# Optimization experiments

Hardware: AMD Instinct MI355X
Metric: run time of the kernel (lower is better)

Reference implementation:

```python
import jax, jax.numpy as jnp
import numpy as np

T = 1_000_000          # number of t_eval points (~1 year at 30 s)
N_ROOMS = 10
N = 12                 # 2 latent wall nodes + n_rooms
DT = 30.0              # seconds between t_eval points
LOAD_SCALE = 50.0      # physical_cooling_scaling: W/m^2 scale for sigmoid(loads)


def setup_inputs() -> dict:
    key = jax.random.key(0)
    k1, k2, k3, k4, k5 = jax.random.split(key, 5)
    t_eval = jnp.arange(T, dtype=jnp.float32) * DT
    x0 = 26.0 * jnp.ones((N,), jnp.float32)  # reset_iv: 26 C at every node
    # Stable slow RC dynamics: negative-definite-ish A with small coupling
    A = (-1e-5 * jnp.eye(N, dtype=jnp.float32)
         + 1e-6 * jax.random.normal(k1, (N, N), jnp.float32))
    B = 1e-6 * jax.random.normal(k2, (N, 1 + N_ROOMS), jnp.float32)
    Tout_data = 10.0 + 20.0 * jax.random.uniform(k3, (T,), jnp.float32)  # outdoor temp samples on t_eval grid
    loads_raw = jax.random.normal(k4, (2, N_ROOMS), jnp.float32)         # pre-sigmoid [cool; gain] loads
    room_areas = 10.0 + 40.0 * jax.random.uniform(k5, (N_ROOMS,), jnp.float32)
    return {"t_eval": t_eval, "x0": x0, "A": A, "B": B,
            "Tout_data": Tout_data, "loads_raw": loads_raw, "room_areas": room_areas}


def reference(t_eval, x0, A, B, Tout_data, loads_raw, room_areas):
    # transform + physical scaling of loads (self.transform = sigmoid)
    loads = jax.nn.sigmoid(loads_raw) * LOAD_SCALE
    cool_load, gain_load = loads[0], loads[1]
    action = 0.0  # no cooling policy -> self.action stays 0
    Q_area = -cool_load * action + gain_load            # [n_rooms]
    Q_watts = Q_area * room_areas                        # proportional_heating
    # u = [Tout; Q_watts] so B@u = B[:,0]*Tout + B[:,1:]@Q_watts (Q constant over t)
    b0 = B[:, 0]                                         # [N]
    Bq = B[:, 1:] @ Q_watts                              # [N], constant forcing
    h = t_eval[1] - t_eval[0]                            # uniform step
    # Linear interp of Tout: value at t_i, midpoint t_i+h/2, and t_{i+1}
    To_t = Tout_data[:-1]
    To_n = Tout_data[1:]
    To_m = 0.5 * (To_t + To_n)

    def f(x, To):  # dy/dt = A x + B u
        return A @ x + b0 * To + Bq

    def step(x, tou):
        to_t, to_m, to_n = tou
        k1 = f(x, to_t)
        k2 = f(x + 0.5 * h * k1, to_m)
        k3 = f(x + 0.5 * h * k2, to_m)
        k4 = f(x + h * k3, to_n)
        xn = x + (h / 6.0) * (k1 + 2.0 * k2 + 2.0 * k3 + k4)
        return xn, xn

    _, xs = jax.lax.scan(step, x0, (To_t, To_m, To_n))
    return jnp.concatenate([x0[None, :], xs], axis=0)  # [T, N]
```

## Files before the change

kernel.cpp:

```cpp
#include <hip/hip_runtime.h>
#include <math.h>


#define S_STEPS 999999
#define CH      8
#define BLK     256
#define NB      489
#define NCHUNK  125000
#define LASTFULL 124998

#define OFF_M   0
#define OFF_C   144
#define OFF_AL  156
#define OFF_BE  168
#define OFF_K   192
#define OFF_P2  320
#define OFF_PA  1472
#define OFF_PL  1616
#define OFF_PD  2048
#define NCONS   3200
#define OFF_AGG 3200
#define OFF_FLAG 9072

#define FMA4(Q,a,b,c,d,acc) fmaf((Q).w,(d),fmaf((Q).z,(c),fmaf((Q).y,(b),fmaf((Q).x,(a),(acc)))))

__device__ __forceinline__ void mv_acc(const float* Pf, const float* x, float* y) {
  const float4* P = reinterpret_cast<const float4*>(Pf);
#pragma unroll
  for (int i = 0; i < 12; ++i) {
    float4 a = P[3*i], b = P[3*i+1], c = P[3*i+2];
    y[i] = FMA4(c, x[8],x[9],x[10],x[11],
            FMA4(b, x[4],x[5],x[6],x[7],
             FMA4(a, x[0],x[1],x[2],x[3], y[i])));
  }
}

__device__ __forceinline__ float rowdot(const float* Prow, const float* xv) {
  const float4* P = reinterpret_cast<const float4*>(Prow);
  float4 a = P[0], b = P[1], c = P[2];
  return FMA4(c, xv[8],xv[9],xv[10],xv[11],
          FMA4(b, xv[4],xv[5],xv[6],xv[7],
           FMA4(a, xv[0],xv[1],xv[2],xv[3], 0.f)));
}

__device__ __forceinline__ void fold_chunk(const float* cons,
                                           const float* tos, float* v) {
  const float4* Kq = reinterpret_cast<const float4*>(cons + OFF_K);
  float4 c0=Kq[0], c1=Kq[1], c2=Kq[2];
  v[0]=c0.x; v[1]=c0.y; v[2]=c0.z; v[3]=c0.w;
  v[4]=c1.x; v[5]=c1.y; v[6]=c1.z; v[7]=c1.w;
  v[8]=c2.x; v[9]=c2.y; v[10]=c2.z; v[11]=c2.w;
#pragma unroll
  for (int s = 0; s < 9; ++s) {
    float ts = tos[s];
    float4 ka=Kq[3*(s+1)], kb=Kq[3*(s+1)+1], kc=Kq[3*(s+1)+2];
    v[0]=fmaf(ka.x,ts,v[0]); v[1]=fmaf(ka.y,ts,v[1]); v[2]=fmaf(ka.z,ts,v[2]); v[3]=fmaf(ka.w,ts,v[3]);
    v[4]=fmaf(kb.x,ts,v[4]); v[5]=fmaf(kb.y,ts,v[5]); v[6]=fmaf(kb.z,ts,v[6]); v[7]=fmaf(kb.w,ts,v[7]);
    v[8]=fmaf(kc.x,ts,v[8]); v[9]=fmaf(kc.y,ts,v[9]); v[10]=fmaf(kc.z,ts,v[10]); v[11]=fmaf(kc.w,ts,v[11]);
  }
}

__global__ void __launch_bounds__(512) setup_kernel(
    const float* __restrict__ t_eval, const float* __restrict__ A,
    const float* __restrict__ Bm, const float* __restrict__ loads_raw,
    const float* __restrict__ areas, float* ws) {
  __shared__ double H1[144], H2[144], H3[144], H4[144], Md[144];
  __shared__ double Qa[144], Qb[144];
  __shared__ double C512s[144], C1024s[144], C2048s[144], C4096s[144];
  __shared__ double C8192s[144], C16384s[144], C32768s[144], Pd3s[144];
  __shared__ double cd[12], ald[12], bed[12], b0d[12], bqd[12];
  __shared__ double Vv[3][12], Kd[120];
  int t = threadIdx.x;
  if (t < NB) ((int*)(ws + OFF_FLAG))[t] = 0;
  double h = (double)t_eval[1] - (double)t_eval[0];
  if (t < 144) H1[t] = h * (double)A[t];
  if (t < 12) {
    b0d[t] = (double)Bm[t*11];
    double s = 0.0;
    for (int r = 0; r < 10; ++r) {
      double gq = 50.0 / (1.0 + exp(-(double)loads_raw[10 + r]));
      s += (double)Bm[t*11 + 1 + r] * (gq * (double)areas[r]);
    }
    bqd[t] = s;
  }
  if (t < 120) Kd[t] = 0.0;
  __syncthreads();
  if (t < 144) {
    int i=t/12, j=t%12; double s=0.0;
#pragma unroll
    for (int m = 0; m < 12; ++m) s += H1[i*12+m]*H1[m*12+j];
    H2[t]=s;
  }
  __syncthreads();
  if (t < 288) {
    int w=t/144, e=t%144, i=e/12, j=e%12;
    const double* Bp = w ? H2 : H1;
    double s = 0.0;
#pragma unroll
    for (int m = 0; m < 12; ++m) s += H2[i*12+m]*Bp[m*12+j];
    (w ? H4 : H3)[e] = s;
  }
  __syncthreads();
  if (t < 12) {
    double hb=0,h2b=0,h3b=0,hb0=0,h2b0=0,h3b0=0;
#pragma unroll
    for (int m = 0; m < 12; ++m) {
      hb  += H1[t*12+m]*bqd[m]; h2b  += H2[t*12+m]*bqd[m]; h3b  += H3[t*12+m]*bqd[m];
      hb0 += H1[t*12+m]*b0d[m]; h2b0 += H2[t*12+m]*b0d[m]; h3b0 += H3[t*12+m]*b0d[m];
    }
    double h6 = h / 6.0;
    cd[t]  = h6*(6.0*bqd[t] + 3.0*hb + h2b + 0.25*h3b);
    ald[t] = h6*(3.0*b0d[t] + 2.0*hb0 + 0.75*h2b0 + 0.25*h3b0);
    bed[t] = h6*(3.0*b0d[t] + hb0 + 0.25*h2b0);
    Vv[0][t]=ald[t]; Vv[1][t]=bed[t]; Vv[2][t]=cd[t];
    Kd[96+t] += ald[t]; Kd[108+t] += bed[t]; Kd[t] += cd[t];
  }
  if (t >= 144 && t < 288) {
    int e=t-144, i=e/12, j=e%12;
    Md[e] = (i==j ? 1.0 : 0.0) + H1[e] + 0.5*H2[e] + H3[e]/6.0 + H4[e]/24.0;
  }
  __syncthreads();
  if (t < 144) { ws[OFF_M+t] = (float)Md[t]; Qa[t] = Md[t]; }
  if (t < 12) {
    ws[OFF_C+t]=(float)cd[t]; ws[OFF_AL+t]=(float)ald[t]; ws[OFF_BE+t]=(float)bed[t];
  }
  __syncthreads();
  double* src = Qa; double* dst = Qb;
  for (int r = 1; r <= 15; ++r) {
    double acc = 0.0, ks = 0.0;
    if (t < 144) {
      int i=t/12, j=t%12;
#pragma unroll
      for (int m = 0; m < 12; ++m) acc += src[i*12+m]*src[m*12+j];
    }
    int w=0, i2=0;
    if (r <= 7 && t >= 256 && t < 292) {
      w=(t-256)/12; i2=(t-256)%12;
#pragma unroll
      for (int m = 0; m < 12; ++m) ks += Md[i2*12+m]*Vv[w][m];
    }
    __syncthreads();
    if (t < 144) {
      dst[t] = acc;
      if (r >= 3 && r <= 10) ws[OFF_P2+(r-3)*144+t] = (float)acc;
      if (r == 9)  C512s[t]=acc;
      if (r == 10) C1024s[t]=acc;
      if (r == 11) { C2048s[t]=acc;  ws[OFF_PL+t]       = (float)acc; }
      if (r == 12) { C4096s[t]=acc;  ws[OFF_PL+144+t]   = (float)acc; }
      if (r == 13) { C8192s[t]=acc;  ws[OFF_PD+144+t]   = (float)acc; }
      if (r == 14) { C16384s[t]=acc; ws[OFF_PD+2*144+t] = (float)acc; }
      if (r == 15) { C32768s[t]=acc; ws[OFF_PD+4*144+t] = (float)acc; }
    }
    if (r <= 7 && t >= 256 && t < 292) {
      Vv[w][i2] = ks;
      if (w == 0) Kd[(8-r)*12+i2] += ks;
      else if (w == 1) Kd[(9-r)*12+i2] += ks;
      else Kd[i2] += ks;
    }
    __syncthreads();
    double* tmp = src; src = dst; dst = tmp;
  }
  if (t < 120) ws[OFF_K+t] = (float)Kd[t];
  if (t < 144) ws[OFF_PD+t] = (t % 13 == 0) ? 1.f : 0.f;
  if (t < 432) {
    int w=t/144, e=t%144, i=e/12, j=e%12;
    const double* Ap = (w==0) ? C512s  : ((w==1) ? C2048s : C8192s);
    const double* Bp = (w==0) ? C1024s : ((w==1) ? C4096s : C16384s);
    double s = 0.0;
#pragma unroll
    for (int m = 0; m < 12; ++m) s += Ap[i*12+m]*Bp[m*12+j];
    if (w==0) ws[OFF_PA+e] = (float)s;
    else if (w==1) ws[OFF_PL+2*144+e] = (float)s;
    else { ws[OFF_PD+3*144+e] = (float)s; Pd3s[e] = s; }
  }
  __syncthreads();
  if (t < 432) {
    int w=t/144, e=t%144, i=e/12, j=e%12;
    const double* Ap = (w==0) ? C8192s : ((w==1) ? C16384s : Pd3s);
    double s = 0.0;
#pragma unroll
    for (int m = 0; m < 12; ++m) s += Ap[i*12+m]*C32768s[m*12+j];
    ws[OFF_PD+(5+w)*144+e] = (float)s;
  }
}

__global__ void __launch_bounds__(BLK, 2) fused_scan(
    const float* __restrict__ cons, const float* __restrict__ To,
    const float* __restrict__ x0, float* __restrict__ agg,
    int* __restrict__ flags, float* __restrict__ out) {
  __shared__ __align__(16) float Lc[NCONS];
  __shared__ __align__(16) float Tw[48];
  __shared__ __align__(16) float Ta[24];
  __shared__ __align__(16) float Pw[48];
  __shared__ __align__(16) float lkb[32*12];
  __shared__ __align__(16) float yv[8*12];
  __shared__ __align__(16) float zv[8*12];
  __shared__ __align__(16) float Xs[12];
  __shared__ __align__(16) float Qw[48];
  int k = threadIdx.x, b = blockIdx.x;
  int g = b*BLK + k, base = g*CH;
  bool active = (g < NCHUNK), fullc = (g <= LASTFULL);
  float to_[9];
#pragma unroll
  for (int i = 0; i < 9; ++i) to_[i] = 0.f;
  if (active) {
    const float4* tp = reinterpret_cast<const float4*>(To + base);
    float4 ta = tp[0], tb = tp[1];
    to_[0]=ta.x; to_[1]=ta.y; to_[2]=ta.z; to_[3]=ta.w;
    to_[4]=tb.x; to_[5]=tb.y; to_[6]=tb.z; to_[7]=tb.w;
    to_[8] = fullc ? To[base+8] : 0.f;
  }
  {
    const float4* s4 = reinterpret_cast<const float4*>(cons);
    float4* d4 = reinterpret_cast<float4*>(Lc);
#pragma unroll
    for (int r = 0; r < 4; ++r) {
      int idx = k + r*BLK;
      if (idx < NCONS/4) d4[idx] = s4[idx];
    }
  }
  __syncthreads();
  const float* lc = Lc;
  float v[12];
  if (fullc) fold_chunk(lc, to_, v);
  else {
#pragma unroll
    for (int i = 0; i < 12; ++i) v[i] = 0.f;
  }
  if (g == 0) {
    float xi[12];
#pragma unroll
    for (int i = 0; i < 12; ++i) xi[i] = x0[i];
    mv_acc(lc + OFF_P2, xi, v);
  }
  int j = k & 63, w = k >> 6;
#pragma unroll
  for (int l = 0; l < 6; ++l) {
    int off = 1 << l;
    float nb[12];
#pragma unroll
    for (int i = 0; i < 12; ++i) nb[i] = __shfl_up(v[i], (unsigned)off, 64);
    if (j >= off) mv_acc(lc + OFF_P2 + l*144, nb, v);
  }
  float se[12];
#pragma unroll
  for (int i = 0; i < 12; ++i) {
    float u = __shfl_up(v[i], 1u, 64);
    se[i] = (j == 0) ? 0.f : u;
  }
  if (j == 63) {
#pragma unroll
    for (int i = 0; i < 12; ++i) Tw[w*12 + i] = v[i];
  }
  __syncthreads();
  if (k < 24) {
    int p = k/12, comp = k - p*12;
    Ta[k] = rowdot(lc + OFF_P2 + 6*144 + comp*12, Tw + 2*p*12)
          + Tw[(2*p+1)*12 + comp];
  }
  __syncthreads();
  if (k < 12) {
    float val = rowdot(lc + OFF_P2 + 7*144 + k*12, Ta) + Ta[12 + k];
    __hip_atomic_store(&agg[b*12 + k], val, __ATOMIC_RELAXED,
                       __HIP_MEMORY_SCOPE_AGENT);
  }
  __syncthreads();
  if (k == 0)
    __hip_atomic_store(&flags[b], 1, __ATOMIC_RELEASE,
                       __HIP_MEMORY_SCOPE_AGENT);
  if (k < 32) {
    int src = b - 1 - k;
    if (src >= 0) {
      while (__hip_atomic_load(&flags[src], __ATOMIC_ACQUIRE,
                               __HIP_MEMORY_SCOPE_AGENT) == 0) {
        __builtin_amdgcn_s_sleep(1);
      }
    }
  }
  __syncthreads();
#pragma unroll
  for (int r = 0; r < 2; ++r) {
    int idx = k + r*BLK;
    if (idx < 384) {
      int slot = idx / 12, comp = idx - slot*12;
      int src = b - 1 - slot;
      float acc = 0.f;
      if (src >= 0) {
        int jj = slot & 3;
        const float* ag = agg + src*12;
        acc = (jj == 0) ? ag[comp]
            : rowdot(lc + OFF_PL + (jj-1)*144 + comp*12, ag);
      }
      lkb[idx] = acc;
    }
  }
  __syncthreads();
  if (k < 96) {
    int i = k/12, comp = k - i*12;
    yv[k] = lkb[(4*i)*12+comp] + lkb[(4*i+1)*12+comp]
          + lkb[(4*i+2)*12+comp] + lkb[(4*i+3)*12+comp];
  } else if (k >= 192 && k < 216) {
    int q = k - 192;
    if (q < 12) Pw[q] = 0.f;
    else Pw[q] = Tw[q-12];
  }
  __syncthreads();
  if (k < 96) {
    int i = k/12, comp = k - i*12;
    zv[k] = (i == 0) ? yv[comp]
          : rowdot(lc + OFF_PD + i*144 + comp*12, yv + i*12);
  } else if (k >= 192 && k < 204) {
    int comp = k - 192;
    Pw[24+comp] = rowdot(lc + OFF_P2 + 6*144 + comp*12, Pw+12) + Tw[12+comp];
  }
  __syncthreads();
  if (k < 12) {
    float s = 0.f;
#pragma unroll
    for (int i = 0; i < 8; ++i) s += zv[i*12 + k];
    Xs[k] = s;
  } else if (k >= 192 && k < 204) {
    int comp = k - 192;
    Pw[36+comp] = rowdot(lc + OFF_P2 + 6*144 + comp*12, Pw+24) + Tw[24+comp];
  }
  __syncthreads();
  if (k < 48) {
    int ww = k/12, comp = k - ww*12;
    float acc;
    if (ww == 0) acc = Xs[comp];
    else if (ww == 1) acc = rowdot(lc + OFF_P2 + 6*144 + comp*12, Xs);
    else if (ww == 2) acc = rowdot(lc + OFF_P2 + 7*144 + comp*12, Xs);
    else acc = rowdot(lc + OFF_PA + comp*12, Xs);
    Qw[k] = acc + Pw[k];
  }
  __syncthreads();
  if (!active) return;
  float x[12];
#pragma unroll
  for (int i = 0; i < 12; ++i) x[i] = Qw[w*12 + i];
#pragma unroll
  for (int l = 0; l < 6; ++l) {
    if ((j >> l) & 1) {
      float vn[12];
#pragma unroll
      for (int i = 0; i < 12; ++i) vn[i] = 0.f;
      mv_acc(lc + OFF_P2 + l*144, x, vn);
#pragma unroll
      for (int i = 0; i < 12; ++i) x[i] = vn[i];
    }
  }
#pragma unroll
  for (int i = 0; i < 12; ++i) x[i] += se[i];
  if (b == 0 && k == 0) {
#pragma unroll
    for (int i = 0; i < 12; ++i) x[i] += x0[i];
#pragma unroll
    for (int i = 0; i < 12; ++i) out[i] = x0[i];
  }
  float cv[12], av[12], bv[12];
#pragma unroll
  for (int i = 0; i < 12; ++i) {
    cv[i] = lc[OFF_C + i]; av[i] = lc[OFF_AL + i]; bv[i] = lc[OFF_BE + i];
  }
  const float4* Mq = reinterpret_cast<const float4*>(lc + OFF_M);
#pragma unroll
  for (int s = 0; s < CH; ++s) {
    float tot = to_[s], ton = to_[s+1];
    float xn[12];
#pragma unroll
    for (int i = 0; i < 12; ++i) {
      float4 a = Mq[3*i], bq = Mq[3*i+1], c = Mq[3*i+2];
      xn[i] = FMA4(c, x[8],x[9],x[10],x[11],
               FMA4(bq, x[4],x[5],x[6],x[7],
                FMA4(a, x[0],x[1],x[2],x[3],
                 fmaf(bv[i],ton,fmaf(av[i],tot,cv[i])))));
    }
    int tt = base + s;
    if (tt < S_STEPS) {
      float4* op = reinterpret_cast<float4*>(out + (size_t)(tt+1)*12);
      op[0] = make_float4(xn[0],xn[1],xn[2],xn[3]);
      op[1] = make_float4(xn[4],xn[5],xn[6],xn[7]);
      op[2] = make_float4(xn[8],xn[9],xn[10],xn[11]);
    }
#pragma unroll
    for (int i = 0; i < 12; ++i) x[i] = xn[i];
  }
}

extern "C" void kernel_launch(void* const* d_in, const int* in_sizes, int n_in,
                              void* d_out, int out_size, void* d_ws, size_t ws_size,
                              hipStream_t stream) {
  const float* t_eval    = (const float*)d_in[0];
  const float* x0        = (const float*)d_in[1];
  const float* A         = (const float*)d_in[2];
  const float* B         = (const float*)d_in[3];
  const float* To        = (const float*)d_in[4];
  const float* loads_raw = (const float*)d_in[5];
  const float* areas     = (const float*)d_in[6];
  float* out = (float*)d_out;
  float* ws  = (float*)d_ws;

  setup_kernel<<<1, 512, 0, stream>>>(t_eval, A, B, loads_raw, areas, ws);
  fused_scan<<<NB, BLK, 0, stream>>>(ws, To, x0, ws + OFF_AGG,
                                     (int*)(ws + OFF_FLAG), out);
}
```

Measured before the change: 130.7 us.

## Halve per-thread chunk size to double block count and raise occupancy

Reduces steps per thread from 8 to 4, which doubles the number of chunks and blocks. The power tables in setup, the constant layout and the decoupled lookback window (64 predecessors instead of 32) are all rebuilt to match. Launch bounds rise from 2 to 4 blocks per CU so more waves run concurrently. The cost is more lookback work per block, a larger shared constant table, more flag polling, and longer serial dependency chains across blocks.

```diff
diff --git a/kernel.cpp b/kernel.cpp
--- a/kernel.cpp
+++ b/kernel.cpp
@@ -3,24 +3,24 @@
 
 
 #define S_STEPS 999999
-#define CH      8
+#define CH      4
 #define BLK     256
-#define NB      489
-#define NCHUNK  125000
-#define LASTFULL 124998
+#define NB      977
+#define NCHUNK  250000
+#define LASTFULL 249998
 
 #define OFF_M   0
 #define OFF_C   144
 #define OFF_AL  156
 #define OFF_BE  168
 #define OFF_K   192
-#define OFF_P2  320
-#define OFF_PA  1472
-#define OFF_PL  1616
-#define OFF_PD  2048
-#define NCONS   3200
-#define OFF_AGG 3200
-#define OFF_FLAG 9072
+#define OFF_P2  264
+#define OFF_PA  1416
+#define OFF_PL  1704
+#define OFF_PD  2136
+#define NCONS   4440
+#define OFF_AGG 4440
+#define OFF_FLAG 16164
 
 #define FMA4(Q,a,b,c,d,acc) fmaf((Q).w,(d),fmaf((Q).z,(c),fmaf((Q).y,(b),fmaf((Q).x,(a),(acc)))))
 
@@ -51,7 +51,7 @@
   v[4]=c1.x; v[5]=c1.y; v[6]=c1.z; v[7]=c1.w;
   v[8]=c2.x; v[9]=c2.y; v[10]=c2.z; v[11]=c2.w;
 #pragma unroll
-  for (int s = 0; s < 9; ++s) {
+  for (int s = 0; s < 5; ++s) {
     float ts = tos[s];
     float4 ka=Kq[3*(s+1)], kb=Kq[3*(s+1)+1], kc=Kq[3*(s+1)+2];
     v[0]=fmaf(ka.x,ts,v[0]); v[1]=fmaf(ka.y,ts,v[1]); v[2]=fmaf(ka.z,ts,v[2]); v[3]=fmaf(ka.w,ts,v[3]);
@@ -66,12 +66,14 @@
     const float* __restrict__ areas, float* ws) {
   __shared__ double H1[144], H2[144], H3[144], H4[144], Md[144];
   __shared__ double Qa[144], Qb[144];
-  __shared__ double C512s[144], C1024s[144], C2048s[144], C4096s[144];
-  __shared__ double C8192s[144], C16384s[144], C32768s[144], Pd3s[144];
+  __shared__ double C256s[144], C512s[144], C1024s[144], C2048s[144];
+  __shared__ double Pd1s[144], Pd2s[144], Pd4s[144], Pd8s[144];
+  __shared__ double Pd3s[144], Pd5s[144], Pd6s[144], Pd7s[144];
   __shared__ double cd[12], ald[12], bed[12], b0d[12], bqd[12];
-  __shared__ double Vv[3][12], Kd[120];
+  __shared__ double Vv[3][12], Kd[72];
   int t = threadIdx.x;
-  if (t < NB) ((int*)(ws + OFF_FLAG))[t] = 0;
+  for (int f = t; f < NB; f += 512)
+    ((int*)(ws + OFF_FLAG))[f] = 0;
   double h = (double)t_eval[1] - (double)t_eval[0];
   if (t < 144) H1[t] = h * (double)A[t];
   if (t < 12) {
@@ -83,7 +85,7 @@
     }
     bqd[t] = s;
   }
-  if (t < 120) Kd[t] = 0.0;
+  if (t < 72) Kd[t] = 0.0;
   __syncthreads();
   if (t < 144) {
     int i=t/12, j=t%12; double s=0.0;
@@ -113,7 +115,7 @@
     ald[t] = h6*(3.0*b0d[t] + 2.0*hb0 + 0.75*h2b0 + 0.25*h3b0);
     bed[t] = h6*(3.0*b0d[t] + hb0 + 0.25*h2b0);
     Vv[0][t]=ald[t]; Vv[1][t]=bed[t]; Vv[2][t]=cd[t];
-    Kd[96+t] += ald[t]; Kd[108+t] += bed[t]; Kd[t] += cd[t];
+    Kd[48+t] += ald[t]; Kd[60+t] += bed[t]; Kd[t] += cd[t];
   }
   if (t >= 144 && t < 288) {
     int e=t-144, i=e/12, j=e%12;
@@ -134,7 +136,7 @@
       for (int m = 0; m < 12; ++m) acc += src[i*12+m]*src[m*12+j];
     }
     int w=0, i2=0;
-    if (r <= 7 && t >= 256 && t < 292) {
+    if (r <= 3 && t >= 256 && t < 292) {
       w=(t-256)/12; i2=(t-256)%12;
 #pragma unroll
       for (int m = 0; m < 12; ++m) ks += Md[i2*12+m]*Vv[w][m];
@@ -142,49 +144,75 @@
     __syncthreads();
     if (t < 144) {
       dst[t] = acc;
-      if (r >= 3 && r <= 10) ws[OFF_P2+(r-3)*144+t] = (float)acc;
+      if (r >= 2 && r <= 9) ws[OFF_P2+(r-2)*144+t] = (float)acc;
+      if (r == 8)  C256s[t]=acc;
       if (r == 9)  C512s[t]=acc;
-      if (r == 10) C1024s[t]=acc;
-      if (r == 11) { C2048s[t]=acc;  ws[OFF_PL+t]       = (float)acc; }
-      if (r == 12) { C4096s[t]=acc;  ws[OFF_PL+144+t]   = (float)acc; }
-      if (r == 13) { C8192s[t]=acc;  ws[OFF_PD+144+t]   = (float)acc; }
-      if (r == 14) { C16384s[t]=acc; ws[OFF_PD+2*144+t] = (float)acc; }
-      if (r == 15) { C32768s[t]=acc; ws[OFF_PD+4*144+t] = (float)acc; }
-    }
-    if (r <= 7 && t >= 256 && t < 292) {
+      if (r == 10) { C1024s[t]=acc; ws[OFF_PL+t]        = (float)acc; }
+      if (r == 11) { C2048s[t]=acc; ws[OFF_PL+144+t]    = (float)acc; }
+      if (r == 12) { Pd1s[t]=acc;   ws[OFF_PD+144+t]    = (float)acc; }
+      if (r == 13) { Pd2s[t]=acc;   ws[OFF_PD+2*144+t]  = (float)acc; }
+      if (r == 14) { Pd4s[t]=acc;   ws[OFF_PD+4*144+t]  = (float)acc; }
+      if (r == 15) { Pd8s[t]=acc;   ws[OFF_PD+8*144+t]  = (float)acc; }
+    }
+    if (r <= 3 && t >= 256 && t < 292) {
       Vv[w][i2] = ks;
-      if (w == 0) Kd[(8-r)*12+i2] += ks;
-      else if (w == 1) Kd[(9-r)*12+i2] += ks;
+      if (w == 0) Kd[(4-r)*12+i2] += ks;
+      else if (w == 1) Kd[(5-r)*12+i2] += ks;
       else Kd[i2] += ks;
     }
     __syncthreads();
     double* tmp = src; src = dst; dst = tmp;
   }
-  if (t < 120) ws[OFF_K+t] = (float)Kd[t];
+  if (t < 72) ws[OFF_K+t] = (float)Kd[t];
   if (t < 144) ws[OFF_PD+t] = (t % 13 == 0) ? 1.f : 0.f;
   if (t < 432) {
     int w=t/144, e=t%144, i=e/12, j=e%12;
-    const double* Ap = (w==0) ? C512s  : ((w==1) ? C2048s : C8192s);
-    const double* Bp = (w==0) ? C1024s : ((w==1) ? C4096s : C16384s);
+    const double* Ap = (w==0) ? C256s : ((w==1) ? C1024s : Pd1s);
+    const double* Bp = (w==0) ? C512s : ((w==1) ? C2048s : Pd2s);
     double s = 0.0;
 #pragma unroll
     for (int m = 0; m < 12; ++m) s += Ap[i*12+m]*Bp[m*12+j];
-    if (w==0) ws[OFF_PA+e] = (float)s;
+    if (w==0) ws[OFF_PA+144+e] = (float)s;
     else if (w==1) ws[OFF_PL+2*144+e] = (float)s;
     else { ws[OFF_PD+3*144+e] = (float)s; Pd3s[e] = s; }
   }
   __syncthreads();
   if (t < 432) {
     int w=t/144, e=t%144, i=e/12, j=e%12;
-    const double* Ap = (w==0) ? C8192s : ((w==1) ? C16384s : Pd3s);
-    double s = 0.0;
-#pragma unroll
-    for (int m = 0; m < 12; ++m) s += Ap[i*12+m]*C32768s[m*12+j];
+    const double* Ap = (w==0) ? Pd1s : ((w==1) ? Pd2s : Pd3s);
+    double s = 0.0;
+#pragma unroll
+    for (int m = 0; m < 12; ++m) s += Ap[i*12+m]*Pd4s[m*12+j];
     ws[OFF_PD+(5+w)*144+e] = (float)s;
-  }
-}
-
-__global__ void __launch_bounds__(BLK, 2) fused_scan(
+    (w==0 ? Pd5s : (w==1 ? Pd6s : Pd7s))[e] = s;
+  }
+  __syncthreads();
+  if (t < 432) {
+    int w=t/144, e=t%144, i=e/12, j=e%12;
+    const double* Ap = (w==0) ? Pd1s : ((w==1) ? Pd2s : Pd3s);
+    double s = 0.0;
+#pragma unroll
+    for (int m = 0; m < 12; ++m) s += Ap[i*12+m]*Pd8s[m*12+j];
+    ws[OFF_PD+(9+w)*144+e] = (float)s;
+  }
+  if (t < 432) {
+    int w=t/144, e=t%144, i=e/12, j=e%12;
+    const double* Ap = (w==0) ? Pd4s : ((w==1) ? Pd5s : Pd6s);
+    double s = 0.0;
+#pragma unroll
+    for (int m = 0; m < 12; ++m) s += Ap[i*12+m]*Pd8s[m*12+j];
+    ws[OFF_PD+(12+w)*144+e] = (float)s;
+  }
+  if (t < 144) {
+    int i=t/12, j=t%12;
+    double s = 0.0;
+#pragma unroll
+    for (int m = 0; m < 12; ++m) s += Pd7s[i*12+m]*Pd8s[m*12+j];
+    ws[OFF_PD+15*144+t] = (float)s;
+  }
+}
+
+__global__ void __launch_bounds__(BLK, 4) fused_scan(
     const float* __restrict__ cons, const float* __restrict__ To,
     const float* __restrict__ x0, float* __restrict__ agg,
     int* __restrict__ flags, float* __restrict__ out) {
@@ -192,29 +220,28 @@
   __shared__ __align__(16) float Tw[48];
   __shared__ __align__(16) float Ta[24];
   __shared__ __align__(16) float Pw[48];
-  __shared__ __align__(16) float lkb[32*12];
-  __shared__ __align__(16) float yv[8*12];
-  __shared__ __align__(16) float zv[8*12];
+  __shared__ __align__(16) float lkb[64*12];
+  __shared__ __align__(16) float yv[16*12];
+  __shared__ __align__(16) float zv[16*12];
   __shared__ __align__(16) float Xs[12];
   __shared__ __align__(16) float Qw[48];
   int k = threadIdx.x, b = blockIdx.x;
   int g = b*BLK + k, base = g*CH;
   bool active = (g < NCHUNK), fullc = (g <= LASTFULL);
-  float to_[9];
-#pragma unroll
-  for (int i = 0; i < 9; ++i) to_[i] = 0.f;
+  float to_[5];
+#pragma unroll
+  for (int i = 0; i < 5; ++i) to_[i] = 0.f;
   if (active) {
     const float4* tp = reinterpret_cast<const float4*>(To + base);
-    float4 ta = tp[0], tb = tp[1];
+    float4 ta = tp[0];
     to_[0]=ta.x; to_[1]=ta.y; to_[2]=ta.z; to_[3]=ta.w;
-    to_[4]=tb.x; to_[5]=tb.y; to_[6]=tb.z; to_[7]=tb.w;
-    to_[8] = fullc ? To[base+8] : 0.f;
+    to_[4] = fullc ? To[base+4] : 0.f;
   }
   {
     const float4* s4 = reinterpret_cast<const float4*>(cons);
     float4* d4 = reinterpret_cast<float4*>(Lc);
 #pragma unroll
-    for (int r = 0; r < 4; ++r) {
+    for (int r = 0; r < 5; ++r) {
       int idx = k + r*BLK;
       if (idx < NCONS/4) d4[idx] = s4[idx];
     }
@@ -268,7 +295,7 @@
   if (k == 0)
     __hip_atomic_store(&flags[b], 1, __ATOMIC_RELEASE,
                        __HIP_MEMORY_SCOPE_AGENT);
-  if (k < 32) {
+  if (k < 64) {
     int src = b - 1 - k;
     if (src >= 0) {
       while (__hip_atomic_load(&flags[src], __ATOMIC_ACQUIRE,
@@ -279,33 +306,31 @@
   }
   __syncthreads();
 #pragma unroll
-  for (int r = 0; r < 2; ++r) {
+  for (int r = 0; r < 3; ++r) {
     int idx = k + r*BLK;
-    if (idx < 384) {
-      int slot = idx / 12, comp = idx - slot*12;
-      int src = b - 1 - slot;
-      float acc = 0.f;
-      if (src >= 0) {
-        int jj = slot & 3;
-        const float* ag = agg + src*12;
-        acc = (jj == 0) ? ag[comp]
-            : rowdot(lc + OFF_PL + (jj-1)*144 + comp*12, ag);
-      }
-      lkb[idx] = acc;
-    }
-  }
-  __syncthreads();
-  if (k < 96) {
+    int slot = idx / 12, comp = idx - slot*12;
+    int src = b - 1 - slot;
+    float acc = 0.f;
+    if (src >= 0) {
+      int jj = slot & 3;
+      const float* ag = agg + src*12;
+      acc = (jj == 0) ? ag[comp]
+          : rowdot(lc + OFF_PL + (jj-1)*144 + comp*12, ag);
+    }
+    lkb[idx] = acc;
+  }
+  __syncthreads();
+  if (k < 192) {
     int i = k/12, comp = k - i*12;
     yv[k] = lkb[(4*i)*12+comp] + lkb[(4*i+1)*12+comp]
           + lkb[(4*i+2)*12+comp] + lkb[(4*i+3)*12+comp];
-  } else if (k >= 192 && k < 216) {
+  } else if (k < 216) {
     int q = k - 192;
     if (q < 12) Pw[q] = 0.f;
     else Pw[q] = Tw[q-12];
   }
   __syncthreads();
-  if (k < 96) {
+  if (k < 192) {
     int i = k/12, comp = k - i*12;
     zv[k] = (i == 0) ? yv[comp]
           : rowdot(lc + OFF_PD + i*144 + comp*12, yv + i*12);
@@ -317,7 +342,7 @@
   if (k < 12) {
     float s = 0.f;
 #pragma unroll
-    for (int i = 0; i < 8; ++i) s += zv[i*12 + k];
+    for (int i = 0; i < 16; ++i) s += zv[i*12 + k];
     Xs[k] = s;
   } else if (k >= 192 && k < 204) {
     int comp = k - 192;
@@ -330,7 +355,7 @@
     if (ww == 0) acc = Xs[comp];
     else if (ww == 1) acc = rowdot(lc + OFF_P2 + 6*144 + comp*12, Xs);
     else if (ww == 2) acc = rowdot(lc + OFF_P2 + 7*144 + comp*12, Xs);
-    else acc = rowdot(lc + OFF_PA + comp*12, Xs);
+    else acc = rowdot(lc + OFF_PA + 144 + comp*12, Xs);
     Qw[k] = acc + Pw[k];
   }
   __syncthreads();
@@ -365,7 +390,7 @@
   const float4* Mq = reinterpret_cast<const float4*>(lc + OFF_M);
 #pragma unroll
   for (int s = 0; s < CH; ++s) {
-    float tot = to_[s], ton = to_[s+1];
+    float tot = to_[s], ton = (s < CH-1) ? to_[s+1] : to_[4];
     float xn[12];
 #pragma unroll
     for (int i = 0; i < 12; ++i) {
```

New measurement: 173.8 us. 1.33x slower.

## Fuse setup into scan kernel with staged flag handoff of constants

Applied to the files above, without the earlier changes.

Merges the single-block setup kernel into the scan kernel as block 0, with worker blocks spinning on two magic-valued flags. Workers load the first part of the constants once the early matrix powers are ready, and the rest just before the cross-block lookback. This aims to remove one kernel launch and overlap constant computation with input loading and the local chunk fold. It risks races, because flags are now cleared concurrently with worker use and the magic flags persist across calls.

```diff
diff --git a/kernel.cpp b/kernel.cpp
--- a/kernel.cpp
+++ b/kernel.cpp
@@ -5,7 +5,7 @@
 #define S_STEPS 999999
 #define CH      8
 #define BLK     256
-#define NB      489
+#define NB_W    489
 #define NCHUNK  125000
 #define LASTFULL 124998
 
@@ -19,8 +19,13 @@
 #define OFF_PL  1616
 #define OFF_PD  2048
 #define NCONS   3200
+#define NS1Q    368
+#define NS2Q    432
 #define OFF_AGG 3200
 #define OFF_FLAG 9072
+#define OFF_SFLAG 9568
+#define MAGIC1  0x1357ACE9
+#define MAGIC2  0x2468BDF1
 
 #define FMA4(Q,a,b,c,d,acc) fmaf((Q).w,(d),fmaf((Q).z,(c),fmaf((Q).y,(b),fmaf((Q).x,(a),(acc)))))
 
@@ -60,134 +65,12 @@
   }
 }
 
-__global__ void __launch_bounds__(512) setup_kernel(
+__global__ void __launch_bounds__(BLK, 2) fused_all(
     const float* __restrict__ t_eval, const float* __restrict__ A,
     const float* __restrict__ Bm, const float* __restrict__ loads_raw,
-    const float* __restrict__ areas, float* ws) {
-  __shared__ double H1[144], H2[144], H3[144], H4[144], Md[144];
-  __shared__ double Qa[144], Qb[144];
-  __shared__ double C512s[144], C1024s[144], C2048s[144], C4096s[144];
-  __shared__ double C8192s[144], C16384s[144], C32768s[144], Pd3s[144];
-  __shared__ double cd[12], ald[12], bed[12], b0d[12], bqd[12];
-  __shared__ double Vv[3][12], Kd[120];
-  int t = threadIdx.x;
-  if (t < NB) ((int*)(ws + OFF_FLAG))[t] = 0;
-  double h = (double)t_eval[1] - (double)t_eval[0];
-  if (t < 144) H1[t] = h * (double)A[t];
-  if (t < 12) {
-    b0d[t] = (double)Bm[t*11];
-    double s = 0.0;
-    for (int r = 0; r < 10; ++r) {
-      double gq = 50.0 / (1.0 + exp(-(double)loads_raw[10 + r]));
-      s += (double)Bm[t*11 + 1 + r] * (gq * (double)areas[r]);
-    }
-    bqd[t] = s;
-  }
-  if (t < 120) Kd[t] = 0.0;
-  __syncthreads();
-  if (t < 144) {
-    int i=t/12, j=t%12; double s=0.0;
-#pragma unroll
-    for (int m = 0; m < 12; ++m) s += H1[i*12+m]*H1[m*12+j];
-    H2[t]=s;
-  }
-  __syncthreads();
-  if (t < 288) {
-    int w=t/144, e=t%144, i=e/12, j=e%12;
-    const double* Bp = w ? H2 : H1;
-    double s = 0.0;
-#pragma unroll
-    for (int m = 0; m < 12; ++m) s += H2[i*12+m]*Bp[m*12+j];
-    (w ? H4 : H3)[e] = s;
-  }
-  __syncthreads();
-  if (t < 12) {
-    double hb=0,h2b=0,h3b=0,hb0=0,h2b0=0,h3b0=0;
-#pragma unroll
-    for (int m = 0; m < 12; ++m) {
-      hb  += H1[t*12+m]*bqd[m]; h2b  += H2[t*12+m]*bqd[m]; h3b  += H3[t*12+m]*bqd[m];
-      hb0 += H1[t*12+m]*b0d[m]; h2b0 += H2[t*12+m]*b0d[m]; h3b0 += H3[t*12+m]*b0d[m];
-    }
-    double h6 = h / 6.0;
-    cd[t]  = h6*(6.0*bqd[t] + 3.0*hb + h2b + 0.25*h3b);
-    ald[t] = h6*(3.0*b0d[t] + 2.0*hb0 + 0.75*h2b0 + 0.25*h3b0);
-    bed[t] = h6*(3.0*b0d[t] + hb0 + 0.25*h2b0);
-    Vv[0][t]=ald[t]; Vv[1][t]=bed[t]; Vv[2][t]=cd[t];
-    Kd[96+t] += ald[t]; Kd[108+t] += bed[t]; Kd[t] += cd[t];
-  }
-  if (t >= 144 && t < 288) {
-    int e=t-144, i=e/12, j=e%12;
-    Md[e] = (i==j ? 1.0 : 0.0) + H1[e] + 0.5*H2[e] + H3[e]/6.0 + H4[e]/24.0;
-  }
-  __syncthreads();
-  if (t < 144) { ws[OFF_M+t] = (float)Md[t]; Qa[t] = Md[t]; }
-  if (t < 12) {
-    ws[OFF_C+t]=(float)cd[t]; ws[OFF_AL+t]=(float)ald[t]; ws[OFF_BE+t]=(float)bed[t];
-  }
-  __syncthreads();
-  double* src = Qa; double* dst = Qb;
-  for (int r = 1; r <= 15; ++r) {
-    double acc = 0.0, ks = 0.0;
-    if (t < 144) {
-      int i=t/12, j=t%12;
-#pragma unroll
-      for (int m = 0; m < 12; ++m) acc += src[i*12+m]*src[m*12+j];
-    }
-    int w=0, i2=0;
-    if (r <= 7 && t >= 256 && t < 292) {
-      w=(t-256)/12; i2=(t-256)%12;
-#pragma unroll
-      for (int m = 0; m < 12; ++m) ks += Md[i2*12+m]*Vv[w][m];
-    }
-    __syncthreads();
-    if (t < 144) {
-      dst[t] = acc;
-      if (r >= 3 && r <= 10) ws[OFF_P2+(r-3)*144+t] = (float)acc;
-      if (r == 9)  C512s[t]=acc;
-      if (r == 10) C1024s[t]=acc;
-      if (r == 11) { C2048s[t]=acc;  ws[OFF_PL+t]       = (float)acc; }
-      if (r == 12) { C4096s[t]=acc;  ws[OFF_PL+144+t]   = (float)acc; }
-      if (r == 13) { C8192s[t]=acc;  ws[OFF_PD+144+t]   = (float)acc; }
-      if (r == 14) { C16384s[t]=acc; ws[OFF_PD+2*144+t] = (float)acc; }
-      if (r == 15) { C32768s[t]=acc; ws[OFF_PD+4*144+t] = (float)acc; }
-    }
-    if (r <= 7 && t >= 256 && t < 292) {
-      Vv[w][i2] = ks;
-      if (w == 0) Kd[(8-r)*12+i2] += ks;
-      else if (w == 1) Kd[(9-r)*12+i2] += ks;
-      else Kd[i2] += ks;
-    }
-    __syncthreads();
-    double* tmp = src; src = dst; dst = tmp;
-  }
-  if (t < 120) ws[OFF_K+t] = (float)Kd[t];
-  if (t < 144) ws[OFF_PD+t] = (t % 13 == 0) ? 1.f : 0.f;
-  if (t < 432) {
-    int w=t/144, e=t%144, i=e/12, j=e%12;
-    const double* Ap = (w==0) ? C512s  : ((w==1) ? C2048s : C8192s);
-    const double* Bp = (w==0) ? C1024s : ((w==1) ? C4096s : C16384s);
-    double s = 0.0;
-#pragma unroll
-    for (int m = 0; m < 12; ++m) s += Ap[i*12+m]*Bp[m*12+j];
-    if (w==0) ws[OFF_PA+e] = (float)s;
-    else if (w==1) ws[OFF_PL+2*144+e] = (float)s;
-    else { ws[OFF_PD+3*144+e] = (float)s; Pd3s[e] = s; }
-  }
-  __syncthreads();
-  if (t < 432) {
-    int w=t/144, e=t%144, i=e/12, j=e%12;
-    const double* Ap = (w==0) ? C8192s : ((w==1) ? C16384s : Pd3s);
-    double s = 0.0;
-#pragma unroll
-    for (int m = 0; m < 12; ++m) s += Ap[i*12+m]*C32768s[m*12+j];
-    ws[OFF_PD+(5+w)*144+e] = (float)s;
-  }
-}
-
-__global__ void __launch_bounds__(BLK, 2) fused_scan(
-    const float* __restrict__ cons, const float* __restrict__ To,
-    const float* __restrict__ x0, float* __restrict__ agg,
-    int* __restrict__ flags, float* __restrict__ out) {
+    const float* __restrict__ areas,
+    float* ws, const float* __restrict__ To,
+    const float* __restrict__ x0, float* __restrict__ out) {
   __shared__ __align__(16) float Lc[NCONS];
   __shared__ __align__(16) float Tw[48];
   __shared__ __align__(16) float Ta[24];
@@ -197,7 +80,142 @@
   __shared__ __align__(16) float zv[8*12];
   __shared__ __align__(16) float Xs[12];
   __shared__ __align__(16) float Qw[48];
-  int k = threadIdx.x, b = blockIdx.x;
+  __shared__ double H1[144], H2[144], H3[144], H4[144], Md[144];
+  __shared__ double Qa[144], Qb[144];
+  __shared__ double C512s[144], C1024s[144], C2048s[144], C4096s[144];
+  __shared__ double C8192s[144], C16384s[144], C32768s[144], Pd3s[144];
+  __shared__ double cd[12], ald[12], bed[12], b0d[12], bqd[12];
+  __shared__ double Vv[3][12], Kd[120];
+
+  int k = threadIdx.x;
+  float* agg   = ws + OFF_AGG;
+  int*   flags = (int*)(ws + OFF_FLAG);
+  int*   sflag = (int*)(ws + OFF_SFLAG);
+
+  if (blockIdx.x == 0) {
+    int t = k;
+    for (int f = t; f < NB_W; f += BLK) flags[f] = 0;
+    double h = (double)t_eval[1] - (double)t_eval[0];
+    if (t < 144) H1[t] = h * (double)A[t];
+    if (t < 12) {
+      b0d[t] = (double)Bm[t*11];
+      double s = 0.0;
+      for (int r = 0; r < 10; ++r) {
+        double gq = 50.0 / (1.0 + exp(-(double)loads_raw[10 + r]));
+        s += (double)Bm[t*11 + 1 + r] * (gq * (double)areas[r]);
+      }
+      bqd[t] = s;
+    }
+    if (t < 120) Kd[t] = 0.0;
+    __syncthreads();
+    if (t < 144) {
+      int i=t/12, j=t%12; double s=0.0;
+#pragma unroll
+      for (int m = 0; m < 12; ++m) s += H1[i*12+m]*H1[m*12+j];
+      H2[t]=s;
+    }
+    __syncthreads();
+    for (int e2 = t; e2 < 288; e2 += BLK) {
+      int w=e2/144, e=e2%144, i=e/12, j=e%12;
+      const double* Bp = w ? H2 : H1;
+      double s = 0.0;
+#pragma unroll
+      for (int m = 0; m < 12; ++m) s += H2[i*12+m]*Bp[m*12+j];
+      (w ? H4 : H3)[e] = s;
+    }
+    __syncthreads();
+    if (t < 12) {
+      double hb=0,h2b=0,h3b=0,hb0=0,h2b0=0,h3b0=0;
+#pragma unroll
+      for (int m = 0; m < 12; ++m) {
+        hb  += H1[t*12+m]*bqd[m]; h2b  += H2[t*12+m]*bqd[m]; h3b  += H3[t*12+m]*bqd[m];
+        hb0 += H1[t*12+m]*b0d[m]; h2b0 += H2[t*12+m]*b0d[m]; h3b0 += H3[t*12+m]*b0d[m];
+      }
+      double h6 = h / 6.0;
+      cd[t]  = h6*(6.0*bqd[t] + 3.0*hb + h2b + 0.25*h3b);
+      ald[t] = h6*(3.0*b0d[t] + 2.0*hb0 + 0.75*h2b0 + 0.25*h3b0);
+      bed[t] = h6*(3.0*b0d[t] + hb0 + 0.25*h2b0);
+      Vv[0][t]=ald[t]; Vv[1][t]=bed[t]; Vv[2][t]=cd[t];
+      Kd[96+t] += ald[t]; Kd[108+t] += bed[t]; Kd[t] += cd[t];
+    }
+    if (t < 144) {
+      int i=t/12, j=t%12;
+      Md[t] = (i==j ? 1.0 : 0.0) + H1[t] + 0.5*H2[t] + H3[t]/6.0 + H4[t]/24.0;
+    }
+    __syncthreads();
+    if (t < 144) { ws[OFF_M+t] = (float)Md[t]; Qa[t] = Md[t]; }
+    if (t < 12) {
+      ws[OFF_C+t]=(float)cd[t]; ws[OFF_AL+t]=(float)ald[t]; ws[OFF_BE+t]=(float)bed[t];
+    }
+    __syncthreads();
+    double* src = Qa; double* dst = Qb;
+    for (int r = 1; r <= 15; ++r) {
+      double acc = 0.0, ks = 0.0;
+      if (t < 144) {
+        int i=t/12, j=t%12;
+#pragma unroll
+        for (int m = 0; m < 12; ++m) acc += src[i*12+m]*src[m*12+j];
+      }
+      int w=0, i2=0;
+      if (r <= 7 && t >= 144 && t < 180) {
+        w=(t-144)/12; i2=(t-144)%12;
+#pragma unroll
+        for (int m = 0; m < 12; ++m) ks += Md[i2*12+m]*Vv[w][m];
+      }
+      __syncthreads();
+      if (t < 144) {
+        dst[t] = acc;
+        if (r >= 3 && r <= 8) ws[OFF_P2+(r-3)*144+t] = (float)acc;
+        if (r == 9)  { ws[OFF_P2+6*144+t] = (float)acc; C512s[t]=acc; }
+        if (r == 10) { ws[OFF_P2+7*144+t] = (float)acc; C1024s[t]=acc; }
+        if (r == 11) { ws[OFF_PL+t]       = (float)acc; C2048s[t]=acc; }
+        if (r == 12) { ws[OFF_PL+144+t]   = (float)acc; C4096s[t]=acc; }
+        if (r == 13) { ws[OFF_PD+144+t]   = (float)acc; C8192s[t]=acc; }
+        if (r == 14) { ws[OFF_PD+2*144+t] = (float)acc; C16384s[t]=acc; }
+        if (r == 15) { ws[OFF_PD+4*144+t] = (float)acc; C32768s[t]=acc; }
+        if (r == 8)  ws[OFF_PD+t] = (t % 13 == 0) ? 1.f : 0.f;
+      }
+      if (r <= 7 && t >= 144 && t < 180) {
+        Vv[w][i2] = ks;
+        if (w == 0) Kd[(8-r)*12+i2] += ks;
+        else if (w == 1) Kd[(9-r)*12+i2] += ks;
+        else Kd[i2] += ks;
+      }
+      if (r == 8 && t < 120) ws[OFF_K+t] = (float)Kd[t];
+      __syncthreads();
+      double* tmp = src; src = dst; dst = tmp;
+      if (r == 10 && t == 0)
+        __hip_atomic_store(&sflag[0], MAGIC1, __ATOMIC_RELEASE,
+                           __HIP_MEMORY_SCOPE_AGENT);
+    }
+    for (int idx = t; idx < 432; idx += BLK) {
+      int w=idx/144, e=idx%144, i=e/12, j=e%12;
+      const double* Ap = (w==0) ? C512s  : ((w==1) ? C2048s : C8192s);
+      const double* Bp = (w==0) ? C1024s : ((w==1) ? C4096s : C16384s);
+      double s = 0.0;
+#pragma unroll
+      for (int m = 0; m < 12; ++m) s += Ap[i*12+m]*Bp[m*12+j];
+      if (w==0) ws[OFF_PA+e] = (float)s;
+      else if (w==1) ws[OFF_PL+2*144+e] = (float)s;
+      else { ws[OFF_PD+3*144+e] = (float)s; Pd3s[e] = s; }
+    }
+    __syncthreads();
+    for (int idx = t; idx < 432; idx += BLK) {
+      int w=idx/144, e=idx%144, i=e/12, j=e%12;
+      const double* Ap = (w==0) ? C8192s : ((w==1) ? C16384s : Pd3s);
+      double s = 0.0;
+#pragma unroll
+      for (int m = 0; m < 12; ++m) s += Ap[i*12+m]*C32768s[m*12+j];
+      ws[OFF_PD+(5+w)*144+e] = (float)s;
+    }
+    __syncthreads();
+    if (t == 0)
+      __hip_atomic_store(&sflag[1], MAGIC2, __ATOMIC_RELEASE,
+                         __HIP_MEMORY_SCOPE_AGENT);
+    return;
+  }
+
+  int b = blockIdx.x - 1;
   int g = b*BLK + k, base = g*CH;
   bool active = (g < NCHUNK), fullc = (g <= LASTFULL);
   float to_[9];
@@ -210,13 +228,21 @@
     to_[4]=tb.x; to_[5]=tb.y; to_[6]=tb.z; to_[7]=tb.w;
     to_[8] = fullc ? To[base+8] : 0.f;
   }
+  if (k == 0) {
+    while (__hip_atomic_load(&sflag[0], __ATOMIC_RELAXED,
+                             __HIP_MEMORY_SCOPE_AGENT) != MAGIC1)
+      __builtin_amdgcn_s_sleep(8);
+    (void)__hip_atomic_load(&sflag[0], __ATOMIC_ACQUIRE,
+                            __HIP_MEMORY_SCOPE_AGENT);
+  }
+  __syncthreads();
   {
-    const float4* s4 = reinterpret_cast<const float4*>(cons);
+    const float4* s4 = reinterpret_cast<const float4*>(ws);
     float4* d4 = reinterpret_cast<float4*>(Lc);
 #pragma unroll
-    for (int r = 0; r < 4; ++r) {
+    for (int r = 0; r < 2; ++r) {
       int idx = k + r*BLK;
-      if (idx < NCONS/4) d4[idx] = s4[idx];
+      if (idx < NS1Q) d4[idx] = s4[idx];
     }
   }
   __syncthreads();
@@ -275,6 +301,22 @@
                                __HIP_MEMORY_SCOPE_AGENT) == 0) {
         __builtin_amdgcn_s_sleep(1);
       }
+    }
+  } else if (k == 32) {
+    while (__hip_atomic_load(&sflag[1], __ATOMIC_RELAXED,
+                             __HIP_MEMORY_SCOPE_AGENT) != MAGIC2)
+      __builtin_amdgcn_s_sleep(2);
+    (void)__hip_atomic_load(&sflag[1], __ATOMIC_ACQUIRE,
+                            __HIP_MEMORY_SCOPE_AGENT);
+  }
+  __syncthreads();
+  {
+    const float4* s4 = reinterpret_cast<const float4*>(ws);
+    float4* d4 = reinterpret_cast<float4*>(Lc);
+#pragma unroll
+    for (int r = 0; r < 2; ++r) {
+      int idx = k + r*BLK;
+      if (idx < NS2Q) d4[NS1Q + idx] = s4[NS1Q + idx];
     }
   }
   __syncthreads();
@@ -400,7 +442,6 @@
   float* out = (float*)d_out;
   float* ws  = (float*)d_ws;
 
-  setup_kernel<<<1, 512, 0, stream>>>(t_eval, A, B, loads_raw, areas, ws);
-  fused_scan<<<NB, BLK, 0, stream>>>(ws, To, x0, ws + OFF_AGG,
-                                     (int*)(ws + OFF_FLAG), out);
+  fused_all<<<NB_W + 1, BLK, 0, stream>>>(t_eval, A, B, loads_raw, areas,
+                                          ws, To, x0, out);
 }
```

Result: no change. 133.2 us (+1.9%).

## Halve per-thread chunk length and double block size in fused scan

Applied to the files above, without the earlier changes.

Each thread now handles 4 steps instead of 8, and blocks grow to 512 threads, so the 489 blocks cover 250000 chunks. The in-block tree combine gains an extra level (Ta1/Ta2, Pa/Pb), and the precomputed power tables are reshaped to match. Large look-back and prefix matrices are now read from global memory rather than staged in LDS, which shrinks LDS use and allows 4 blocks per CU. The aim is more parallelism and a shorter serial recurrence per thread, at the cost of more combine stages, more barriers, and global loads in the look-back phase.

```diff
diff --git a/kernel.cpp b/kernel.cpp
--- a/kernel.cpp
+++ b/kernel.cpp
@@ -3,24 +3,23 @@
 
 
 #define S_STEPS 999999
-#define CH      8
-#define BLK     256
+#define CH      4
+#define BLK     512
 #define NB      489
-#define NCHUNK  125000
-#define LASTFULL 124998
+#define NCHUNK  250000
+#define LASTFULL 249998
 
 #define OFF_M   0
 #define OFF_C   144
 #define OFF_AL  156
 #define OFF_BE  168
 #define OFF_K   192
-#define OFF_P2  320
-#define OFF_PA  1472
-#define OFF_PL  1616
-#define OFF_PD  2048
-#define NCONS   3200
-#define OFF_AGG 3200
-#define OFF_FLAG 9072
+#define OFF_P2  264
+#define NLC     1560
+#define OFF_PL  1560
+#define OFF_PD  1992
+#define OFF_AGG 3144
+#define OFF_FLAG 9012
 
 #define FMA4(Q,a,b,c,d,acc) fmaf((Q).w,(d),fmaf((Q).z,(c),fmaf((Q).y,(b),fmaf((Q).x,(a),(acc)))))
 
@@ -51,7 +50,7 @@
   v[4]=c1.x; v[5]=c1.y; v[6]=c1.z; v[7]=c1.w;
   v[8]=c2.x; v[9]=c2.y; v[10]=c2.z; v[11]=c2.w;
 #pragma unroll
-  for (int s = 0; s < 9; ++s) {
+  for (int s = 0; s < 5; ++s) {
     float ts = tos[s];
     float4 ka=Kq[3*(s+1)], kb=Kq[3*(s+1)+1], kc=Kq[3*(s+1)+2];
     v[0]=fmaf(ka.x,ts,v[0]); v[1]=fmaf(ka.y,ts,v[1]); v[2]=fmaf(ka.z,ts,v[2]); v[3]=fmaf(ka.w,ts,v[3]);
@@ -66,10 +65,10 @@
     const float* __restrict__ areas, float* ws) {
   __shared__ double H1[144], H2[144], H3[144], H4[144], Md[144];
   __shared__ double Qa[144], Qb[144];
-  __shared__ double C512s[144], C1024s[144], C2048s[144], C4096s[144];
-  __shared__ double C8192s[144], C16384s[144], C32768s[144], Pd3s[144];
+  __shared__ double C2048s[144], C4096s[144], C8192s[144];
+  __shared__ double C16384s[144], C32768s[144], Pd3s[144];
   __shared__ double cd[12], ald[12], bed[12], b0d[12], bqd[12];
-  __shared__ double Vv[3][12], Kd[120];
+  __shared__ double Vv[3][12], Kd[72];
   int t = threadIdx.x;
   if (t < NB) ((int*)(ws + OFF_FLAG))[t] = 0;
   double h = (double)t_eval[1] - (double)t_eval[0];
@@ -83,7 +82,7 @@
     }
     bqd[t] = s;
   }
-  if (t < 120) Kd[t] = 0.0;
+  if (t < 72) Kd[t] = 0.0;
   __syncthreads();
   if (t < 144) {
     int i=t/12, j=t%12; double s=0.0;
@@ -113,7 +112,7 @@
     ald[t] = h6*(3.0*b0d[t] + 2.0*hb0 + 0.75*h2b0 + 0.25*h3b0);
     bed[t] = h6*(3.0*b0d[t] + hb0 + 0.25*h2b0);
     Vv[0][t]=ald[t]; Vv[1][t]=bed[t]; Vv[2][t]=cd[t];
-    Kd[96+t] += ald[t]; Kd[108+t] += bed[t]; Kd[t] += cd[t];
+    Kd[48+t] += ald[t]; Kd[60+t] += bed[t]; Kd[t] += cd[t];
   }
   if (t >= 144 && t < 288) {
     int e=t-144, i=e/12, j=e%12;
@@ -134,7 +133,7 @@
       for (int m = 0; m < 12; ++m) acc += src[i*12+m]*src[m*12+j];
     }
     int w=0, i2=0;
-    if (r <= 7 && t >= 256 && t < 292) {
+    if (r <= 3 && t >= 256 && t < 292) {
       w=(t-256)/12; i2=(t-256)%12;
 #pragma unroll
       for (int m = 0; m < 12; ++m) ks += Md[i2*12+m]*Vv[w][m];
@@ -142,35 +141,35 @@
     __syncthreads();
     if (t < 144) {
       dst[t] = acc;
-      if (r >= 3 && r <= 10) ws[OFF_P2+(r-3)*144+t] = (float)acc;
-      if (r == 9)  C512s[t]=acc;
-      if (r == 10) C1024s[t]=acc;
-      if (r == 11) { C2048s[t]=acc;  ws[OFF_PL+t]       = (float)acc; }
-      if (r == 12) { C4096s[t]=acc;  ws[OFF_PL+144+t]   = (float)acc; }
-      if (r == 13) { C8192s[t]=acc;  ws[OFF_PD+144+t]   = (float)acc; }
-      if (r == 14) { C16384s[t]=acc; ws[OFF_PD+2*144+t] = (float)acc; }
-      if (r == 15) { C32768s[t]=acc; ws[OFF_PD+4*144+t] = (float)acc; }
-    }
-    if (r <= 7 && t >= 256 && t < 292) {
+      if (r >= 2 && r <= 7) ws[OFF_P2+(r-2)*144+t] = (float)acc;
+      if (r == 8)  { ws[OFF_P2+6*144+t] = (float)acc;
+                     ws[OFF_PD+t] = (t % 13 == 0) ? 1.f : 0.f; }
+      if (r == 9)  ws[OFF_P2+7*144+t] = (float)acc;
+      if (r == 10) ws[OFF_P2+8*144+t] = (float)acc;
+      if (r == 11) { ws[OFF_PL+t]       = (float)acc; C2048s[t]=acc; }
+      if (r == 12) { ws[OFF_PL+144+t]   = (float)acc; C4096s[t]=acc; }
+      if (r == 13) { ws[OFF_PD+144+t]   = (float)acc; C8192s[t]=acc; }
+      if (r == 14) { ws[OFF_PD+2*144+t] = (float)acc; C16384s[t]=acc; }
+      if (r == 15) { ws[OFF_PD+4*144+t] = (float)acc; C32768s[t]=acc; }
+    }
+    if (r <= 3 && t >= 256 && t < 292) {
       Vv[w][i2] = ks;
-      if (w == 0) Kd[(8-r)*12+i2] += ks;
-      else if (w == 1) Kd[(9-r)*12+i2] += ks;
+      if (w == 0) Kd[(4-r)*12+i2] += ks;
+      else if (w == 1) Kd[(5-r)*12+i2] += ks;
       else Kd[i2] += ks;
     }
     __syncthreads();
     double* tmp = src; src = dst; dst = tmp;
   }
-  if (t < 120) ws[OFF_K+t] = (float)Kd[t];
-  if (t < 144) ws[OFF_PD+t] = (t % 13 == 0) ? 1.f : 0.f;
-  if (t < 432) {
+  if (t < 72) ws[OFF_K+t] = (float)Kd[t];
+  if (t < 288) {
     int w=t/144, e=t%144, i=e/12, j=e%12;
-    const double* Ap = (w==0) ? C512s  : ((w==1) ? C2048s : C8192s);
-    const double* Bp = (w==0) ? C1024s : ((w==1) ? C4096s : C16384s);
+    const double* Ap = (w==0) ? C2048s : C8192s;
+    const double* Bp = (w==0) ? C4096s : C16384s;
     double s = 0.0;
 #pragma unroll
     for (int m = 0; m < 12; ++m) s += Ap[i*12+m]*Bp[m*12+j];
-    if (w==0) ws[OFF_PA+e] = (float)s;
-    else if (w==1) ws[OFF_PL+2*144+e] = (float)s;
+    if (w==0) ws[OFF_PL+2*144+e] = (float)s;
     else { ws[OFF_PD+3*144+e] = (float)s; Pd3s[e] = s; }
   }
   __syncthreads();
@@ -184,40 +183,37 @@
   }
 }
 
-__global__ void __launch_bounds__(BLK, 2) fused_scan(
+__global__ void __launch_bounds__(BLK, 4) fused_scan(
     const float* __restrict__ cons, const float* __restrict__ To,
     const float* __restrict__ x0, float* __restrict__ agg,
     int* __restrict__ flags, float* __restrict__ out) {
-  __shared__ __align__(16) float Lc[NCONS];
-  __shared__ __align__(16) float Tw[48];
-  __shared__ __align__(16) float Ta[24];
-  __shared__ __align__(16) float Pw[48];
+  __shared__ __align__(16) float Lc[NLC];
+  __shared__ __align__(16) float Tw[96];
+  __shared__ __align__(16) float Ta1[48];
+  __shared__ __align__(16) float Ta2[24];
+  __shared__ __align__(16) float Pa[96], Pb[96];
   __shared__ __align__(16) float lkb[32*12];
   __shared__ __align__(16) float yv[8*12];
   __shared__ __align__(16) float zv[8*12];
   __shared__ __align__(16) float Xs[12];
-  __shared__ __align__(16) float Qw[48];
+  __shared__ __align__(16) float Sq[96];
+  __shared__ __align__(16) float Qw[96];
   int k = threadIdx.x, b = blockIdx.x;
   int g = b*BLK + k, base = g*CH;
   bool active = (g < NCHUNK), fullc = (g <= LASTFULL);
-  float to_[9];
-#pragma unroll
-  for (int i = 0; i < 9; ++i) to_[i] = 0.f;
+  float to_[5];
+#pragma unroll
+  for (int i = 0; i < 5; ++i) to_[i] = 0.f;
   if (active) {
     const float4* tp = reinterpret_cast<const float4*>(To + base);
-    float4 ta = tp[0], tb = tp[1];
+    float4 ta = tp[0];
     to_[0]=ta.x; to_[1]=ta.y; to_[2]=ta.z; to_[3]=ta.w;
-    to_[4]=tb.x; to_[5]=tb.y; to_[6]=tb.z; to_[7]=tb.w;
-    to_[8] = fullc ? To[base+8] : 0.f;
+    to_[4] = fullc ? To[base+4] : 0.f;
   }
   {
     const float4* s4 = reinterpret_cast<const float4*>(cons);
     float4* d4 = reinterpret_cast<float4*>(Lc);
-#pragma unroll
-    for (int r = 0; r < 4; ++r) {
-      int idx = k + r*BLK;
-      if (idx < NCONS/4) d4[idx] = s4[idx];
-    }
+    if (k < NLC/4) d4[k] = s4[k];
   }
   __syncthreads();
   const float* lc = Lc;
@@ -253,16 +249,34 @@
     for (int i = 0; i < 12; ++i) Tw[w*12 + i] = v[i];
   }
   __syncthreads();
+  if (k < 48) {
+    int q = k/12, comp = k - q*12;
+    Ta1[k] = rowdot(lc + OFF_P2 + 6*144 + comp*12, Tw + 2*q*12)
+           + Tw[(2*q+1)*12 + comp];
+  } else if (k >= 96 && k < 192) {
+    int idx = k - 96, wv = idx/12, comp = idx - wv*12;
+    Pa[idx] = (wv == 0) ? Tw[idx]
+            : rowdot(lc + OFF_P2 + 6*144 + comp*12, Tw + (wv-1)*12) + Tw[idx];
+  }
+  __syncthreads();
   if (k < 24) {
     int p = k/12, comp = k - p*12;
-    Ta[k] = rowdot(lc + OFF_P2 + 6*144 + comp*12, Tw + 2*p*12)
-          + Tw[(2*p+1)*12 + comp];
+    Ta2[k] = rowdot(lc + OFF_P2 + 7*144 + comp*12, Ta1 + 2*p*12)
+           + Ta1[(2*p+1)*12 + comp];
+  } else if (k >= 96 && k < 192) {
+    int idx = k - 96, wv = idx/12, comp = idx - wv*12;
+    Pb[idx] = (wv < 2) ? Pa[idx]
+            : rowdot(lc + OFF_P2 + 7*144 + comp*12, Pa + (wv-2)*12) + Pa[idx];
   }
   __syncthreads();
   if (k < 12) {
-    float val = rowdot(lc + OFF_P2 + 7*144 + k*12, Ta) + Ta[12 + k];
+    float val = rowdot(lc + OFF_P2 + 8*144 + k*12, Ta2) + Ta2[12 + k];
     __hip_atomic_store(&agg[b*12 + k], val, __ATOMIC_RELAXED,
                        __HIP_MEMORY_SCOPE_AGENT);
+  } else if (k >= 96 && k < 192) {
+    int idx = k - 96, wv = idx/12, comp = idx - wv*12;
+    Pa[idx] = (wv < 4) ? Pb[idx]
+            : rowdot(lc + OFF_P2 + 8*144 + comp*12, Pb + (wv-4)*12) + Pb[idx];
   }
   __syncthreads();
   if (k == 0)
@@ -278,40 +292,29 @@
     }
   }
   __syncthreads();
-#pragma unroll
-  for (int r = 0; r < 2; ++r) {
-    int idx = k + r*BLK;
-    if (idx < 384) {
-      int slot = idx / 12, comp = idx - slot*12;
-      int src = b - 1 - slot;
-      float acc = 0.f;
-      if (src >= 0) {
-        int jj = slot & 3;
-        const float* ag = agg + src*12;
-        acc = (jj == 0) ? ag[comp]
-            : rowdot(lc + OFF_PL + (jj-1)*144 + comp*12, ag);
-      }
-      lkb[idx] = acc;
-    }
+  if (k < 384) {
+    int slot = k / 12, comp = k - slot*12;
+    int src = b - 1 - slot;
+    float acc = 0.f;
+    if (src >= 0) {
+      int jj = slot & 3;
+      const float* ag = agg + src*12;
+      acc = (jj == 0) ? ag[comp]
+          : rowdot(cons + OFF_PL + (jj-1)*144 + comp*12, ag);
+    }
+    lkb[k] = acc;
   }
   __syncthreads();
   if (k < 96) {
     int i = k/12, comp = k - i*12;
     yv[k] = lkb[(4*i)*12+comp] + lkb[(4*i+1)*12+comp]
           + lkb[(4*i+2)*12+comp] + lkb[(4*i+3)*12+comp];
-  } else if (k >= 192 && k < 216) {
-    int q = k - 192;
-    if (q < 12) Pw[q] = 0.f;
-    else Pw[q] = Tw[q-12];
   }
   __syncthreads();
   if (k < 96) {
     int i = k/12, comp = k - i*12;
     zv[k] = (i == 0) ? yv[comp]
-          : rowdot(lc + OFF_PD + i*144 + comp*12, yv + i*12);
-  } else if (k >= 192 && k < 204) {
-    int comp = k - 192;
-    Pw[24+comp] = rowdot(lc + OFF_P2 + 6*144 + comp*12, Pw+12) + Tw[12+comp];
+          : rowdot(cons + OFF_PD + i*144 + comp*12, yv + i*12);
   }
   __syncthreads();
   if (k < 12) {
@@ -319,19 +322,26 @@
 #pragma unroll
     for (int i = 0; i < 8; ++i) s += zv[i*12 + k];
     Xs[k] = s;
-  } else if (k >= 192 && k < 204) {
-    int comp = k - 192;
-    Pw[36+comp] = rowdot(lc + OFF_P2 + 6*144 + comp*12, Pw+24) + Tw[24+comp];
+  }
+  __syncthreads();
+  if (k < 12) {
+    Sq[k] = Xs[k];
+    Sq[12 + k] = rowdot(lc + OFF_P2 + 6*144 + k*12, Xs);
+  }
+  __syncthreads();
+  if (k < 24) {
+    int q = k/12, comp = k - q*12;
+    Sq[(2+q)*12 + comp] = rowdot(lc + OFF_P2 + 7*144 + comp*12, Sq + q*12);
   }
   __syncthreads();
   if (k < 48) {
-    int ww = k/12, comp = k - ww*12;
-    float acc;
-    if (ww == 0) acc = Xs[comp];
-    else if (ww == 1) acc = rowdot(lc + OFF_P2 + 6*144 + comp*12, Xs);
-    else if (ww == 2) acc = rowdot(lc + OFF_P2 + 7*144 + comp*12, Xs);
-    else acc = rowdot(lc + OFF_PA + comp*12, Xs);
-    Qw[k] = acc + Pw[k];
+    int q = k/12, comp = k - q*12;
+    Sq[(4+q)*12 + comp] = rowdot(lc + OFF_P2 + 8*144 + comp*12, Sq + q*12);
+  }
+  __syncthreads();
+  if (k < 96) {
+    int wv = k/12;
+    Qw[k] = Sq[k] + ((wv == 0) ? 0.f : Pa[k - 12]);
   }
   __syncthreads();
   if (!active) return;
@@ -365,7 +375,7 @@
   const float4* Mq = reinterpret_cast<const float4*>(lc + OFF_M);
 #pragma unroll
   for (int s = 0; s < CH; ++s) {
-    float tot = to_[s], ton = to_[s+1];
+    float tot = to_[s], ton = (s < CH-1) ? to_[s+1] : to_[4];
     float xn[12];
 #pragma unroll
     for (int i = 0; i < 12; ++i) {
```

After: 161.4 us. 23.5% more time.
